# Optimization experiments

Hardware: AMD Instinct MI355X
Metric: run time of the kernel (lower is better)

Reference implementation:

```python
import jax, jax.numpy as jnp
import numpy as np

K = 8          # max_output_degree (complete 8-ary tree)
DEPTH = 7      # number of levels
LEVEL_OFFS = [(K**l - 1) // (K - 1) for l in range(DEPTH + 1)]  # [0,1,9,73,...]
N = LEVEL_OFFS[DEPTH]  # 299593 nodes
V, X, H, O = 32000, 128, 128, 128


def setup_inputs() -> dict:
    key = jax.random.key(0)
    ks = jax.random.split(key, 7)
    x = jax.random.randint(ks[0], (N,), 0, V, dtype=jnp.int32)
    mask = jnp.ones((N,), dtype=jnp.int32)
    # children of node i are K*i+1 .. K*i+K; out-of-range -> sentinel N (zero pad row)
    ch = np.arange(N, dtype=np.int64)[:, None] * K + 1 + np.arange(K, dtype=np.int64)[None, :]
    children = jnp.asarray(np.where(ch < N, ch, N).astype(np.int32))
    s = 0.02
    emb = jax.random.normal(ks[1], (V, X), dtype=jnp.float32) * s
    W_in = jax.random.normal(ks[2], (X, H), dtype=jnp.float32) * s
    b_in = jnp.zeros((H,), dtype=jnp.float32)
    U = jax.random.normal(ks[3], (H, H), dtype=jnp.float32) * s
    W_out = jax.random.normal(ks[4], (H, O), dtype=jnp.float32) * s
    b_out = jnp.zeros((O,), dtype=jnp.float32)
    return {"x": x, "mask": mask, "children": children, "emb": emb,
            "W_in": W_in, "b_in": b_in, "U": U, "W_out": W_out, "b_out": b_out}


def reference(x, mask, children, emb, W_in, b_in, U, b_out=None, W_out=None, **_):
    # keyword-safe wrapper not used; real signature below
    raise NotImplementedError


def reference(x, mask, children, emb, W_in, b_in, U, W_out, b_out):
    mf = mask.astype(jnp.float32)[:, None]                 # [N,1]
    embeds = emb[x * mask]                                 # [N,X] input_module(x*mask)
    h_input = (embeds @ W_in + b_in) * mf                  # [N,H] W_in(embeds)*mask
    h = jnp.zeros((N + 1, h_input.shape[1]), dtype=h_input.dtype)  # row N = zero pad
    # bottom-up topological propagation, level by level
    for l in range(DEPTH - 1, -1, -1):
        s, e = LEVEL_OFFS[l], LEVEL_OFFS[l + 1]
        if l == DEPTH - 1:
            # leaves: no children messages
            h_new = jnp.tanh(h_input[s:e])
        else:
            h_ch = h[children[s:e]]                        # [n_l,K,H] gather child states
            agg = h_ch.sum(axis=1) @ U                     # SumChild aggregator + linear
            h_new = jnp.tanh(h_input[s:e] + agg)           # apply_node_func
        h = h.at[s:e].set(h_new)
    out = h[:N] @ W_out + b_out                            # output_module
    return out
```

## Files before the change

kernel.cpp:

```cpp
#include <hip/hip_runtime.h>
#include <hip/hip_bf16.h>


typedef __bf16 bf16x8 __attribute__((ext_vector_type(8)));
typedef float f32x4 __attribute__((ext_vector_type(4)));
typedef float f32x2 __attribute__((ext_vector_type(2)));
typedef unsigned short ushort8 __attribute__((ext_vector_type(8)));

#define NNODES 299593

static __device__ __forceinline__ unsigned short f2bf(float f) {
  union { float f; unsigned int u; } v; v.f = f;
  unsigned int u = v.u;
  u += 0x7fff + ((u >> 16) & 1);
  return (unsigned short)(u >> 16);
}

static __device__ __forceinline__ unsigned int pk2bf(float a, float b) {
#if __has_builtin(__builtin_amdgcn_cvt_pk_bf16_f32)
  typedef __bf16 bf16x2 __attribute__((ext_vector_type(2)));
  union { bf16x2 v; unsigned int u; } c;
  c.v = __builtin_amdgcn_cvt_pk_bf16_f32(a, b);
  return c.u;
#else
  return (unsigned int)f2bf(a) | ((unsigned int)f2bf(b) << 16);
#endif
}

static __device__ __forceinline__ float fast_tanh(float x) {
  float y = x * 2.885390081777927f;
#if __has_builtin(__builtin_amdgcn_exp2f)
  float e = __builtin_amdgcn_exp2f(y);
#else
  float e = __builtin_exp2f(y);
#endif
#if __has_builtin(__builtin_amdgcn_rcpf)
  float r = __builtin_amdgcn_rcpf(e + 1.0f);
#else
  float r = 1.0f / (e + 1.0f);
#endif
  return __builtin_fmaf(-2.0f, r, 1.0f);
}

__global__ void prep_weights(const float* __restrict__ W_in,
                             const float* __restrict__ U,
                             const float* __restrict__ W_out,
                             unsigned short* __restrict__ w_sw) {
  int f = blockIdx.x * 256 + threadIdx.x;
  int m = f >> 14;
  int r = f & 16383;
  int j = r & 7;
  int lane = (r >> 3) & 63;
  int nt = (r >> 9) & 7;
  int kt = (r >> 12) & 3;
  int k = kt * 32 + ((lane >> 4) * 8) + j;
  int n = nt * 16 + (lane & 15);
  const float* W = (m == 0) ? W_in : (m == 1) ? U : W_out;
  w_sw[f] = f2bf(W[k * 128 + n]);
}

static __device__ __forceinline__ void gemm16(f32x4 acc[8],
    const unsigned short* a_base, const unsigned short* b_sw, int lane) {
  const int coll = lane & 15;
  const int quad = lane >> 4;
#pragma unroll
  for (int kt = 0; kt < 4; ++kt) {
    bf16x8 a = *(const bf16x8*)(a_base + coll * 136 + kt * 32 + quad * 8);
#pragma unroll
    for (int nt = 0; nt < 8; ++nt) {
      bf16x8 b = *(const bf16x8*)(b_sw + (((kt * 8 + nt) * 64 + lane) * 8));
      acc[nt] = __builtin_amdgcn_mfma_f32_16x16x32_bf16(a, b, acc[nt], 0, 0, 0);
    }
  }
}

template <bool LEAF>
static __device__ __forceinline__ void tile_body(
    const int* __restrict__ x, const int* __restrict__ mask,
    const float* __restrict__ emb, const float* __restrict__ b_in,
    const float* __restrict__ b_out, const unsigned short* __restrict__ w_sw,
    unsigned short* __restrict__ h, float* __restrict__ out,
    int e, int row0, unsigned short (*Abuf)[136], int tid) {
  const int lane = tid & 63;
  const int wave = tid >> 6;

  {
    const int r = tid >> 2;
    const int cg = tid & 3;
    const int grow = row0 + r;
    const int valid = (grow < e);
    const int m = valid ? mask[grow] : 0;
    const int idx = valid ? x[grow] * m : 0;
    const float fm = (float)m;
    const float* erow = emb + (size_t)idx * 128 + cg * 32;
#pragma unroll
    for (int b = 0; b < 4; ++b) {
      f32x4 v0 = *(const f32x4*)(erow + b * 8);
      f32x4 v1 = *(const f32x4*)(erow + b * 8 + 4);
      union { ushort8 s; unsigned int u[4]; } w;
      w.u[0] = pk2bf(v0[0] * fm, v0[1] * fm);
      w.u[1] = pk2bf(v0[2] * fm, v0[3] * fm);
      w.u[2] = pk2bf(v1[0] * fm, v1[1] * fm);
      w.u[3] = pk2bf(v1[2] * fm, v1[3] * fm);
      *(ushort8*)&Abuf[r][cg * 32 + b * 8] = w.s;
    }
  }
  __builtin_amdgcn_wave_barrier();

  f32x4 acc[8];
#pragma unroll
  for (int nt = 0; nt < 8; ++nt) acc[nt] = (f32x4){0.f, 0.f, 0.f, 0.f};
  gemm16(acc, &Abuf[wave * 16][0], w_sw, lane);

  if (!LEAF) {
    const int r = tid >> 2;
    const int cg = tid & 3;
    const int grow = row0 + r;
    f32x2 sums[16];
#pragma unroll
    for (int q = 0; q < 16; ++q) sums[q] = (f32x2){0.f, 0.f};
    if (grow < e) {
      const unsigned short* hp = h + ((size_t)grow * 8 + 1) * 128 + cg * 32;
#pragma unroll
      for (int j = 0; j < 8; ++j) {
#pragma unroll
        for (int b = 0; b < 2; ++b) {
          union { ushort8 s; unsigned int u[4]; } hv;
          hv.s = *(const ushort8*)(hp + j * 128 + b * 16);
#pragma unroll
          for (int q = 0; q < 4; ++q) {
            union { unsigned int u; float f; } lo, hi;
            lo.u = hv.u[q] << 16;
            hi.u = hv.u[q] & 0xffff0000u;
            sums[b * 8 + q] += (f32x2){lo.f, hi.f};
          }
          hv.s = *(const ushort8*)(hp + j * 128 + b * 16 + 8);
#pragma unroll
          for (int q = 0; q < 4; ++q) {
            union { unsigned int u; float f; } lo, hi;
            lo.u = hv.u[q] << 16;
            hi.u = hv.u[q] & 0xffff0000u;
            sums[b * 8 + 4 + q] += (f32x2){lo.f, hi.f};
          }
        }
      }
    }
#pragma unroll
    for (int b = 0; b < 2; ++b) {
      union { ushort8 s; unsigned int u[4]; } w0, w1;
#pragma unroll
      for (int q = 0; q < 4; ++q) {
        w0.u[q] = pk2bf(sums[b * 8 + q][0], sums[b * 8 + q][1]);
        w1.u[q] = pk2bf(sums[b * 8 + 4 + q][0], sums[b * 8 + 4 + q][1]);
      }
      *(ushort8*)&Abuf[r][cg * 32 + b * 16] = w0.s;
      *(ushort8*)&Abuf[r][cg * 32 + b * 16 + 8] = w1.s;
    }
    __builtin_amdgcn_wave_barrier();
    gemm16(acc, &Abuf[wave * 16][0], w_sw + 16384, lane);
  }

  const int coll = lane & 15;
  const int quad = lane >> 4;
  float binv[8];
#pragma unroll
  for (int nt = 0; nt < 8; ++nt) binv[nt] = b_in[nt * 16 + coll];
#pragma unroll
  for (int r2 = 0; r2 < 4; ++r2) {
    const int rowl = wave * 16 + quad * 4 + r2;
    const int grow = row0 + rowl;
    const float mval = (grow < e) ? (float)mask[grow] : 0.f;
#pragma unroll
    for (int nt = 0; nt < 8; ++nt) {
      float t = acc[nt][r2] + mval * binv[nt];
      Abuf[rowl][nt * 16 + coll] = f2bf(fast_tanh(t));
    }
  }
  __builtin_amdgcn_wave_barrier();

  {
    const int sr = wave * 16 + (lane >> 2);
    const int sc = (lane & 3) * 8;
    const int grow = row0 + sr;
    if (grow < e) {
      unsigned short* hp = h + (size_t)grow * 128;
#pragma unroll
      for (int i = 0; i < 4; ++i)
        *(ushort8*)(hp + sc + i * 32) = *(const ushort8*)&Abuf[sr][sc + i * 32];
    }
  }

  f32x4 oacc[8];
#pragma unroll
  for (int nt = 0; nt < 8; ++nt) oacc[nt] = (f32x4){0.f, 0.f, 0.f, 0.f};
  gemm16(oacc, &Abuf[wave * 16][0], w_sw + 32768, lane);

  float boutv[8];
#pragma unroll
  for (int nt = 0; nt < 8; ++nt) boutv[nt] = b_out[nt * 16 + coll];
#pragma unroll
  for (int r2 = 0; r2 < 4; ++r2) {
    const int rowl = wave * 16 + quad * 4 + r2;
    const int grow = row0 + rowl;
    if (grow < e) {
#pragma unroll
      for (int nt = 0; nt < 8; ++nt)
        out[(size_t)grow * 128 + nt * 16 + coll] = oacc[nt][r2] + boutv[nt];
    }
  }
}

template <bool LEAF>
__global__ __launch_bounds__(256) void level_kernel(
    const int* __restrict__ x, const int* __restrict__ mask,
    const float* __restrict__ emb, const float* __restrict__ b_in,
    const float* __restrict__ b_out, const unsigned short* __restrict__ w_sw,
    unsigned short* __restrict__ h, float* __restrict__ out, int s, int e) {
  __shared__ __align__(16) unsigned short Abuf[64][136];
  tile_body<LEAF>(x, mask, emb, b_in, b_out, w_sw, h, out, e,
                  s + blockIdx.x * 64, Abuf, threadIdx.x);
}

__global__ __launch_bounds__(256) void tail_kernel(
    const int* __restrict__ x, const int* __restrict__ mask,
    const float* __restrict__ emb, const float* __restrict__ b_in,
    const float* __restrict__ b_out, const unsigned short* __restrict__ w_sw,
    unsigned short* __restrict__ h, float* __restrict__ out) {
  __shared__ __align__(16) unsigned short Abuf[64][136];
  tile_body<false>(x, mask, emb, b_in, b_out, w_sw, h, out, 73, 9, Abuf,
                   threadIdx.x);
  __syncthreads();
  tile_body<false>(x, mask, emb, b_in, b_out, w_sw, h, out, 9, 1, Abuf,
                   threadIdx.x);
  __syncthreads();
  tile_body<false>(x, mask, emb, b_in, b_out, w_sw, h, out, 1, 0, Abuf,
                   threadIdx.x);
}

extern "C" void kernel_launch(void* const* d_in, const int* in_sizes, int n_in,
                              void* d_out, int out_size, void* d_ws,
                              size_t ws_size, hipStream_t stream) {
  const int* x = (const int*)d_in[0];
  const int* mask = (const int*)d_in[1];
  const float* emb = (const float*)d_in[3];
  const float* W_in = (const float*)d_in[4];
  const float* b_in = (const float*)d_in[5];
  const float* U = (const float*)d_in[6];
  const float* W_out = (const float*)d_in[7];
  const float* b_out = (const float*)d_in[8];
  float* out = (float*)d_out;

  unsigned short* h = (unsigned short*)d_ws;
  unsigned short* w_sw = h + (size_t)NNODES * 128;

  prep_weights<<<192, 256, 0, stream>>>(W_in, U, W_out, w_sw);

  level_kernel<true><<<4096, 256, 0, stream>>>(x, mask, emb, b_in, b_out, w_sw,
                                               h, out, 37449, 299593);
  level_kernel<false><<<512, 256, 0, stream>>>(x, mask, emb, b_in, b_out, w_sw,
                                               h, out, 4681, 37449);
  level_kernel<false><<<64, 256, 0, stream>>>(x, mask, emb, b_in, b_out, w_sw,
                                              h, out, 585, 4681);
  level_kernel<false><<<8, 256, 0, stream>>>(x, mask, emb, b_in, b_out, w_sw,
                                             h, out, 73, 585);
  tail_kernel<<<1, 256, 0, stream>>>(x, mask, emb, b_in, b_out, w_sw, h, out);
}
```

Baseline: 314.2 us.

## Gather embeddings into MFMA registers and software-pipeline two leaf tiles per block

The embedding gather now loads each lane's slice straight into MFMA A-fragment registers instead of staging it through LDS. A dedicated leaf kernel processes two 64-row tiles per block and issues the second tile's embedding gather before computing the first, to hide gather latency. Bias vectors are loaded once per kernel, the mask is fetched once and broadcast with a shuffle, and bounds checks are compiled out for levels whose sizes divide evenly. This halves the leaf grid, which lowers parallelism and raises register pressure in exchange for the overlap.

```diff
diff --git a/kernel.cpp b/kernel.cpp
--- a/kernel.cpp
+++ b/kernel.cpp
@@ -59,7 +59,50 @@
   w_sw[f] = f2bf(W[k * 128 + n]);
 }
 
-static __device__ __forceinline__ void gemm16(f32x4 acc[8],
+union U8 { ushort8 s; bf16x8 v; unsigned int u[4]; };
+
+struct Raw { f32x4 p[8]; float fm; };
+
+static __device__ __forceinline__ void gather_issue(Raw& r, const int* x,
+    const int* mask, const float* emb, int row, int valid, int quad) {
+  int m = 0, idx = 0;
+  if (valid) { m = mask[row]; idx = x[row] * m; }
+  r.fm = (float)m;
+  const float* er = emb + (size_t)idx * 128 + quad * 8;
+#pragma unroll
+  for (int kt = 0; kt < 4; ++kt) {
+    r.p[kt * 2]     = *(const f32x4*)(er + kt * 32);
+    r.p[kt * 2 + 1] = *(const f32x4*)(er + kt * 32 + 4);
+  }
+}
+
+static __device__ __forceinline__ void cvt_af(bf16x8 af[4], const Raw& r) {
+  const float fm = r.fm;
+#pragma unroll
+  for (int kt = 0; kt < 4; ++kt) {
+    U8 w;
+    f32x4 a = r.p[kt * 2], b = r.p[kt * 2 + 1];
+    w.u[0] = pk2bf(a[0] * fm, a[1] * fm);
+    w.u[1] = pk2bf(a[2] * fm, a[3] * fm);
+    w.u[2] = pk2bf(b[0] * fm, b[1] * fm);
+    w.u[3] = pk2bf(b[2] * fm, b[3] * fm);
+    af[kt] = w.v;
+  }
+}
+
+static __device__ __forceinline__ void gemm_reg(f32x4 acc[8],
+    const bf16x8 af[4], const unsigned short* b_sw, int lane) {
+#pragma unroll
+  for (int kt = 0; kt < 4; ++kt)
+#pragma unroll
+    for (int nt = 0; nt < 8; ++nt) {
+      bf16x8 b = *(const bf16x8*)(b_sw + (((kt * 8 + nt) * 64 + lane) * 8));
+      acc[nt] = __builtin_amdgcn_mfma_f32_16x16x32_bf16(af[kt], b, acc[nt],
+                                                        0, 0, 0);
+    }
+}
+
+static __device__ __forceinline__ void gemm_lds(f32x4 acc[8],
     const unsigned short* a_base, const unsigned short* b_sw, int lane) {
   const int coll = lane & 15;
   const int quad = lane >> 4;
@@ -74,58 +117,34 @@
   }
 }
 
-template <bool LEAF>
-static __device__ __forceinline__ void tile_body(
-    const int* __restrict__ x, const int* __restrict__ mask,
-    const float* __restrict__ emb, const float* __restrict__ b_in,
-    const float* __restrict__ b_out, const unsigned short* __restrict__ w_sw,
+template <bool LEAF, bool BOUNDS>
+static __device__ __forceinline__ void tile_core(
+    const bf16x8 af[4], float fm, int row0w, int e, const unsigned short* w_sw,
     unsigned short* __restrict__ h, float* __restrict__ out,
-    int e, int row0, unsigned short (*Abuf)[136], int tid) {
-  const int lane = tid & 63;
-  const int wave = tid >> 6;
-
-  {
-    const int r = tid >> 2;
-    const int cg = tid & 3;
-    const int grow = row0 + r;
-    const int valid = (grow < e);
-    const int m = valid ? mask[grow] : 0;
-    const int idx = valid ? x[grow] * m : 0;
-    const float fm = (float)m;
-    const float* erow = emb + (size_t)idx * 128 + cg * 32;
-#pragma unroll
-    for (int b = 0; b < 4; ++b) {
-      f32x4 v0 = *(const f32x4*)(erow + b * 8);
-      f32x4 v1 = *(const f32x4*)(erow + b * 8 + 4);
-      union { ushort8 s; unsigned int u[4]; } w;
-      w.u[0] = pk2bf(v0[0] * fm, v0[1] * fm);
-      w.u[1] = pk2bf(v0[2] * fm, v0[3] * fm);
-      w.u[2] = pk2bf(v1[0] * fm, v1[1] * fm);
-      w.u[3] = pk2bf(v1[2] * fm, v1[3] * fm);
-      *(ushort8*)&Abuf[r][cg * 32 + b * 8] = w.s;
-    }
-  }
-  __builtin_amdgcn_wave_barrier();
+    unsigned short (*Aw)[136], int lane, const float* binv,
+    const float* boutv) {
+  const int coll = lane & 15;
+  const int quad = lane >> 4;
 
   f32x4 acc[8];
 #pragma unroll
   for (int nt = 0; nt < 8; ++nt) acc[nt] = (f32x4){0.f, 0.f, 0.f, 0.f};
-  gemm16(acc, &Abuf[wave * 16][0], w_sw, lane);
+  gemm_reg(acc, af, w_sw, lane);
 
   if (!LEAF) {
-    const int r = tid >> 2;
-    const int cg = tid & 3;
-    const int grow = row0 + r;
+    const int r = lane >> 2;
+    const int cg = lane & 3;
+    const int grow = row0w + r;
     f32x2 sums[16];
 #pragma unroll
     for (int q = 0; q < 16; ++q) sums[q] = (f32x2){0.f, 0.f};
-    if (grow < e) {
+    if (!BOUNDS || grow < e) {
       const unsigned short* hp = h + ((size_t)grow * 8 + 1) * 128 + cg * 32;
 #pragma unroll
       for (int j = 0; j < 8; ++j) {
 #pragma unroll
         for (int b = 0; b < 2; ++b) {
-          union { ushort8 s; unsigned int u[4]; } hv;
+          U8 hv;
           hv.s = *(const ushort8*)(hp + j * 128 + b * 16);
 #pragma unroll
           for (int q = 0; q < 4; ++q) {
@@ -147,78 +166,132 @@
     }
 #pragma unroll
     for (int b = 0; b < 2; ++b) {
-      union { ushort8 s; unsigned int u[4]; } w0, w1;
+      U8 w0, w1;
 #pragma unroll
       for (int q = 0; q < 4; ++q) {
         w0.u[q] = pk2bf(sums[b * 8 + q][0], sums[b * 8 + q][1]);
         w1.u[q] = pk2bf(sums[b * 8 + 4 + q][0], sums[b * 8 + 4 + q][1]);
       }
-      *(ushort8*)&Abuf[r][cg * 32 + b * 16] = w0.s;
-      *(ushort8*)&Abuf[r][cg * 32 + b * 16 + 8] = w1.s;
+      *(ushort8*)&Aw[r][cg * 32 + b * 16] = w0.s;
+      *(ushort8*)&Aw[r][cg * 32 + b * 16 + 8] = w1.s;
     }
     __builtin_amdgcn_wave_barrier();
-    gemm16(acc, &Abuf[wave * 16][0], w_sw + 16384, lane);
-  }
-
+    gemm_lds(acc, &Aw[0][0], w_sw + 16384, lane);
+    __builtin_amdgcn_wave_barrier();
+  }
+
+#pragma unroll
+  for (int r2 = 0; r2 < 4; ++r2) {
+    const int rowl = quad * 4 + r2;
+    const float mval = __shfl(fm, rowl);
+#pragma unroll
+    for (int nt = 0; nt < 8; ++nt) {
+      float t = acc[nt][r2] + mval * binv[nt];
+      Aw[rowl][nt * 16 + coll] = f2bf(fast_tanh(t));
+    }
+  }
+  __builtin_amdgcn_wave_barrier();
+
+  {
+    const int sr = lane >> 2;
+    const int sc = (lane & 3) * 8;
+    const int grow = row0w + sr;
+    if (!BOUNDS || grow < e) {
+      unsigned short* hp = h + (size_t)grow * 128;
+#pragma unroll
+      for (int i = 0; i < 4; ++i)
+        *(ushort8*)(hp + sc + i * 32) = *(const ushort8*)&Aw[sr][sc + i * 32];
+    }
+  }
+
+#pragma unroll
+  for (int nt = 0; nt < 8; ++nt) acc[nt] = (f32x4){0.f, 0.f, 0.f, 0.f};
+  gemm_lds(acc, &Aw[0][0], w_sw + 32768, lane);
+
+#pragma unroll
+  for (int r2 = 0; r2 < 4; ++r2) {
+    const int grow = row0w + quad * 4 + r2;
+    if (!BOUNDS || grow < e) {
+#pragma unroll
+      for (int nt = 0; nt < 8; ++nt)
+        out[(size_t)grow * 128 + nt * 16 + coll] = acc[nt][r2] + boutv[nt];
+    }
+  }
+}
+
+template <bool BOUNDS>
+static __device__ __forceinline__ void level_body(
+    const int* __restrict__ x, const int* __restrict__ mask,
+    const float* __restrict__ emb, const unsigned short* __restrict__ w_sw,
+    unsigned short* __restrict__ h, float* __restrict__ out, int row0blk,
+    int e, unsigned short (*Abuf)[136], int tid, const float* binv,
+    const float* boutv) {
+  const int lane = tid & 63;
+  const int wave = tid >> 6;
+  const int quad = lane >> 4;
+  const int row0w = row0blk + wave * 16;
+  const int row = row0w + (lane & 15);
+  Raw ra;
+  gather_issue(ra, x, mask, emb, row, !BOUNDS || row < e, quad);
+  bf16x8 af[4];
+  cvt_af(af, ra);
+  tile_core<false, BOUNDS>(af, ra.fm, row0w, e, w_sw, h, out,
+                           (unsigned short(*)[136]) & Abuf[wave * 16], lane,
+                           binv, boutv);
+}
+
+__global__ __launch_bounds__(256) void leaf_kernel(
+    const int* __restrict__ x, const int* __restrict__ mask,
+    const float* __restrict__ emb, const float* __restrict__ b_in,
+    const float* __restrict__ b_out, const unsigned short* __restrict__ w_sw,
+    unsigned short* __restrict__ h, float* __restrict__ out) {
+  __shared__ __align__(16) unsigned short Abuf[64][136];
+  const int tid = threadIdx.x;
+  const int lane = tid & 63;
+  const int wave = tid >> 6;
   const int coll = lane & 15;
   const int quad = lane >> 4;
-  float binv[8];
-#pragma unroll
-  for (int nt = 0; nt < 8; ++nt) binv[nt] = b_in[nt * 16 + coll];
-#pragma unroll
-  for (int r2 = 0; r2 < 4; ++r2) {
-    const int rowl = wave * 16 + quad * 4 + r2;
-    const int grow = row0 + rowl;
-    const float mval = (grow < e) ? (float)mask[grow] : 0.f;
-#pragma unroll
-    for (int nt = 0; nt < 8; ++nt) {
-      float t = acc[nt][r2] + mval * binv[nt];
-      Abuf[rowl][nt * 16 + coll] = f2bf(fast_tanh(t));
-    }
-  }
-  __builtin_amdgcn_wave_barrier();
-
-  {
-    const int sr = wave * 16 + (lane >> 2);
-    const int sc = (lane & 3) * 8;
-    const int grow = row0 + sr;
-    if (grow < e) {
-      unsigned short* hp = h + (size_t)grow * 128;
-#pragma unroll
-      for (int i = 0; i < 4; ++i)
-        *(ushort8*)(hp + sc + i * 32) = *(const ushort8*)&Abuf[sr][sc + i * 32];
-    }
-  }
-
-  f32x4 oacc[8];
-#pragma unroll
-  for (int nt = 0; nt < 8; ++nt) oacc[nt] = (f32x4){0.f, 0.f, 0.f, 0.f};
-  gemm16(oacc, &Abuf[wave * 16][0], w_sw + 32768, lane);
-
-  float boutv[8];
-#pragma unroll
-  for (int nt = 0; nt < 8; ++nt) boutv[nt] = b_out[nt * 16 + coll];
-#pragma unroll
-  for (int r2 = 0; r2 < 4; ++r2) {
-    const int rowl = wave * 16 + quad * 4 + r2;
-    const int grow = row0 + rowl;
-    if (grow < e) {
-#pragma unroll
-      for (int nt = 0; nt < 8; ++nt)
-        out[(size_t)grow * 128 + nt * 16 + coll] = oacc[nt][r2] + boutv[nt];
-    }
-  }
-}
-
-template <bool LEAF>
+  unsigned short(*Aw)[136] = (unsigned short(*)[136]) & Abuf[wave * 16];
+
+  float binv[8], boutv[8];
+#pragma unroll
+  for (int nt = 0; nt < 8; ++nt) {
+    binv[nt] = b_in[nt * 16 + coll];
+    boutv[nt] = b_out[nt * 16 + coll];
+  }
+
+  const int r0w = 37449 + blockIdx.x * 64 + wave * 16;
+  const int r1w = r0w + 2048 * 64;
+
+  Raw ra;
+  gather_issue(ra, x, mask, emb, r0w + coll, 1, quad);
+  bf16x8 af[4];
+  cvt_af(af, ra);
+  Raw rb;
+  gather_issue(rb, x, mask, emb, r1w + coll, 1, quad);
+  tile_core<true, false>(af, ra.fm, r0w, 0, w_sw, h, out, Aw, lane, binv,
+                         boutv);
+  cvt_af(af, rb);
+  tile_core<true, false>(af, rb.fm, r1w, 0, w_sw, h, out, Aw, lane, binv,
+                         boutv);
+}
+
+template <bool BOUNDS>
 __global__ __launch_bounds__(256) void level_kernel(
     const int* __restrict__ x, const int* __restrict__ mask,
     const float* __restrict__ emb, const float* __restrict__ b_in,
     const float* __restrict__ b_out, const unsigned short* __restrict__ w_sw,
     unsigned short* __restrict__ h, float* __restrict__ out, int s, int e) {
   __shared__ __align__(16) unsigned short Abuf[64][136];
-  tile_body<LEAF>(x, mask, emb, b_in, b_out, w_sw, h, out, e,
-                  s + blockIdx.x * 64, Abuf, threadIdx.x);
+  const int coll = threadIdx.x & 15;
+  float binv[8], boutv[8];
+#pragma unroll
+  for (int nt = 0; nt < 8; ++nt) {
+    binv[nt] = b_in[nt * 16 + coll];
+    boutv[nt] = b_out[nt * 16 + coll];
+  }
+  level_body<BOUNDS>(x, mask, emb, w_sw, h, out, s + blockIdx.x * 64, e, Abuf,
+                     threadIdx.x, binv, boutv);
 }
 
 __global__ __launch_bounds__(256) void tail_kernel(
@@ -227,14 +300,21 @@
     const float* __restrict__ b_out, const unsigned short* __restrict__ w_sw,
     unsigned short* __restrict__ h, float* __restrict__ out) {
   __shared__ __align__(16) unsigned short Abuf[64][136];
-  tile_body<false>(x, mask, emb, b_in, b_out, w_sw, h, out, 73, 9, Abuf,
-                   threadIdx.x);
+  const int coll = threadIdx.x & 15;
+  float binv[8], boutv[8];
+#pragma unroll
+  for (int nt = 0; nt < 8; ++nt) {
+    binv[nt] = b_in[nt * 16 + coll];
+    boutv[nt] = b_out[nt * 16 + coll];
+  }
+  level_body<true>(x, mask, emb, w_sw, h, out, 9, 73, Abuf, threadIdx.x, binv,
+                   boutv);
   __syncthreads();
-  tile_body<false>(x, mask, emb, b_in, b_out, w_sw, h, out, 9, 1, Abuf,
-                   threadIdx.x);
+  level_body<true>(x, mask, emb, w_sw, h, out, 1, 9, Abuf, threadIdx.x, binv,
+                   boutv);
   __syncthreads();
-  tile_body<false>(x, mask, emb, b_in, b_out, w_sw, h, out, 1, 0, Abuf,
-                   threadIdx.x);
+  level_body<true>(x, mask, emb, w_sw, h, out, 0, 1, Abuf, threadIdx.x, binv,
+                   boutv);
 }
 
 extern "C" void kernel_launch(void* const* d_in, const int* in_sizes, int n_in,
@@ -255,8 +335,8 @@
 
   prep_weights<<<192, 256, 0, stream>>>(W_in, U, W_out, w_sw);
 
-  level_kernel<true><<<4096, 256, 0, stream>>>(x, mask, emb, b_in, b_out, w_sw,
-                                               h, out, 37449, 299593);
+  leaf_kernel<<<2048, 256, 0, stream>>>(x, mask, emb, b_in, b_out, w_sw, h,
+                                        out);
   level_kernel<false><<<512, 256, 0, stream>>>(x, mask, emb, b_in, b_out, w_sw,
                                                h, out, 4681, 37449);
   level_kernel<false><<<64, 256, 0, stream>>>(x, mask, emb, b_in, b_out, w_sw,
```

Measured after the change: 362.2 us. 15.3% more time.
